# Kernel tuning notes

Hardware: AMD Instinct MI355X
Metric: run time of the kernel (lower is better)

Reference implementation:

```python
import jax, jax.numpy as jnp
import numpy as np
import math

EMBED_DIM = 1024
NUM_HEADS = 16
HEAD_DIM = EMBED_DIM // NUM_HEADS
MAX_LEN = 5000
LN_EPS = 1e-5


def _positional_encoding(max_len, embed_dim):
    pos = np.arange(max_len, dtype=np.float32)[:, None]
    div = np.exp(np.arange(0, embed_dim, 2, dtype=np.float32) * (-math.log(10000.0) / embed_dim))
    pe = np.zeros((max_len, embed_dim), dtype=np.float32)
    pe[:, 0::2] = np.sin(pos * div)
    pe[:, 1::2] = np.cos(pos * div)
    return jnp.asarray(pe)[None]  # [1, max_len, D]


def setup_inputs() -> dict:
    key = jax.random.key(0)
    ks = jax.random.split(key, 12)
    s = 1.0 / math.sqrt(EMBED_DIM)
    D = EMBED_DIM
    return {
        "x": jax.random.normal(ks[0], (4, 2048, D), dtype=jnp.float32),
        "wq": jax.random.uniform(ks[1], (D, D), jnp.float32, -s, s),
        "bq": jax.random.uniform(ks[2], (D,), jnp.float32, -s, s),
        "wk": jax.random.uniform(ks[3], (D, D), jnp.float32, -s, s),
        "bk": jax.random.uniform(ks[4], (D,), jnp.float32, -s, s),
        "wv": jax.random.uniform(ks[5], (D, D), jnp.float32, -s, s),
        "bv": jax.random.uniform(ks[6], (D,), jnp.float32, -s, s),
        "wo": jax.random.uniform(ks[7], (D, D), jnp.float32, -s, s),
        "bo": jax.random.uniform(ks[8], (D,), jnp.float32, -s, s),
        "gamma": jnp.ones((D,), jnp.float32),
        "beta": jnp.zeros((D,), jnp.float32),
        "pe": _positional_encoding(MAX_LEN, D),
    }


def reference(x, wq, bq, wk, bk, wv, bv, wo, bo, gamma, beta, pe):
    B, S, D = x.shape
    H, Hd = NUM_HEADS, HEAD_DIM
    x = x + pe[:, :S, :]
    # projections; weights stored as [in, out]
    q = (x @ wq + bq).reshape(B, S, H, Hd).transpose(0, 2, 1, 3)
    k = (x @ wk + bk).reshape(B, S, H, Hd).transpose(0, 2, 1, 3)
    v = (x @ wv + bv).reshape(B, S, H, Hd).transpose(0, 2, 1, 3)
    scores = jnp.einsum("bhqd,bhkd->bhqk", q, k) / math.sqrt(Hd)
    attn = jax.nn.softmax(scores, axis=-1)  # dropout is identity in eval
    out = jnp.einsum("bhqk,bhkd->bhqd", attn, v)
    out = out.transpose(0, 2, 1, 3).reshape(B, S, D)
    out = out @ wo + bo
    # residual + layernorm
    h = out + x
    mu = jnp.mean(h, axis=-1, keepdims=True)
    var = jnp.var(h, axis=-1, keepdims=True)
    return (h - mu) * jax.lax.rsqrt(var + LN_EPS) * gamma + beta
```

## Files before the change

kernel.cpp:

```cpp
#include <hip/hip_runtime.h>

#define DEV __device__ __forceinline__

typedef __attribute__((ext_vector_type(4))) float floatx4;
typedef __attribute__((ext_vector_type(8))) short short8;

DEV unsigned short f2bf(float f) {
  unsigned u = __float_as_uint(f);
  u += 0x7FFF + ((u >> 16) & 1);
  return (unsigned short)(u >> 16);
}
DEV float bf2f(unsigned short h) { return __uint_as_float(((unsigned)h) << 16); }

DEV unsigned pkbf(float lo, float hi) {
  return __builtin_amdgcn_perm(__float_as_uint(hi) + 0x8000u,
                               __float_as_uint(lo) + 0x8000u, 0x07060302u);
}

#if __has_builtin(__builtin_amdgcn_exp2f)
#define EXP2(x) __builtin_amdgcn_exp2f(x)
#else
#define EXP2(x) exp2f(x)
#endif

#define GLD16(g, l)                                                            \
  __builtin_amdgcn_global_load_lds(                                            \
      (const __attribute__((address_space(1))) void*)(g),                      \
      (__attribute__((address_space(3))) void*)(l), 16, 0, 0)

__global__ void k_prep(const float* __restrict__ x, const float* __restrict__ pe,
                       const float* __restrict__ w0, const float* __restrict__ w1,
                       const float* __restrict__ w2, const float* __restrict__ w3,
                       unsigned short* __restrict__ wt, float* __restrict__ xf,
                       unsigned short* __restrict__ xb) {
  __shared__ float t[64][65];
  const int bid = blockIdx.x, tid = threadIdx.x;
  if (bid < 1024) {
    const int z = bid >> 8, rem = bid & 255;
    const int bx = rem & 15, by = rem >> 4;
    const int tx = tid & 63, ty = tid >> 6;
    const float* wsel = (z == 0) ? w0 : (z == 1) ? w1 : (z == 2) ? w2 : w3;
    unsigned short* out = wt + (size_t)z * 1048576;
    const int k0 = bx * 64, n0 = by * 64;
    for (int i = ty; i < 64; i += 4)
      t[i][tx] = wsel[(size_t)(k0 + i) * 1024 + n0 + tx];
    __syncthreads();
    for (int i = ty; i < 64; i += 4)
      out[(size_t)(n0 + i) * 1024 + k0 + tx] = f2bf(t[tx][i]);
  } else {
    const int idx = (bid - 1024) * 256 + tid;
    const int row = idx >> 8;
    const int c4 = idx & 255;
    const int s = row & 2047;
    const float4 xv = ((const float4*)x)[idx];
    const float4 pv = ((const float4*)pe)[s * 256 + c4];
    float4 r;
    r.x = xv.x + pv.x; r.y = xv.y + pv.y; r.z = xv.z + pv.z; r.w = xv.w + pv.w;
    ((float4*)xf)[idx] = r;
    ushort4 o;
    o.x = f2bf(r.x); o.y = f2bf(r.y); o.z = f2bf(r.z); o.w = f2bf(r.w);
    ((ushort4*)xb)[idx] = o;
  }
}

#define GEMM_CORE(Aptr, Bptr, RB, CB)                                          \
  for (int k0 = 0; k0 < 1024; k0 += 64) {                                      \
    _Pragma("unroll") for (int r = 0; r < 4; ++r) {                            \
      const int c = r * 256 + tid;                                             \
      const int rw = c >> 3;                                                   \
      const int gc = ((c & 7) ^ (rw & 7)) << 3;                                \
      GLD16((Aptr) + (size_t)((RB) + rw) * 1024 + k0 + gc,                     \
            As + (size_t)(r * 256 + wave * 64) * 8);                           \
      GLD16((Bptr) + (size_t)((CB) + rw) * 1024 + k0 + gc,                     \
            Bs + (size_t)(r * 256 + wave * 64) * 8);                           \
    }                                                                          \
    __syncthreads();                                                           \
    _Pragma("unroll") for (int kk = 0; kk < 2; ++kk) {                         \
      short8 fa[4], fb[4];                                                     \
      _Pragma("unroll") for (int i = 0; i < 4; ++i) {                          \
        fa[i] = *(const short8*)(As + (wm * 64 + i * 16 + l16) * 64 +          \
                                 (((kk * 4 + quad) ^ (l16 & 7)) << 3));        \
        fb[i] = *(const short8*)(Bs + (wn * 64 + i * 16 + l16) * 64 +          \
                                 (((kk * 4 + quad) ^ (l16 & 7)) << 3));        \
      }                                                                        \
      _Pragma("unroll") for (int mi = 0; mi < 4; ++mi)                         \
          _Pragma("unroll") for (int ni = 0; ni < 4; ++ni) acc[mi][ni] =       \
          __builtin_amdgcn_mfma_f32_16x16x32_bf16(fa[mi], fb[ni],              \
                                                  acc[mi][ni], 0, 0, 0);       \
    }                                                                          \
    __syncthreads();                                                           \
  }

__global__ __launch_bounds__(256, 4) void k_gemmqkvt(
    const unsigned short* __restrict__ xpeb, const unsigned short* __restrict__ wt,
    const float* __restrict__ bqp, const float* __restrict__ bkp,
    const float* __restrict__ bvp, unsigned short* __restrict__ qb,
    unsigned short* __restrict__ kb, unsigned short* __restrict__ vtb) {
  __shared__ unsigned short As[128 * 64];
  __shared__ unsigned short Bs[128 * 64];
  const int tid = threadIdx.x;
  const int lane = tid & 63, wave = tid >> 6;
  const int quad = lane >> 4, l16 = lane & 15;
  const int wm = wave >> 1, wn = wave & 1;
  const int id = blockIdx.x;

  floatx4 acc[4][4];
  const floatx4 vzero = {0.f, 0.f, 0.f, 0.f};
#pragma unroll
  for (int i = 0; i < 4; ++i)
#pragma unroll
    for (int j = 0; j < 4; ++j) acc[i][j] = vzero;

  if (id < 1024) {
    const int xcd = id & 7, j = id >> 3;
    const int bx = (xcd << 3) | (j & 7), by = j >> 3;
    const int rb = bx * 128, cb = by * 128;
    GEMM_CORE(xpeb, wt, rb, cb);
    const int which = cb >> 10;
    const float* bias = (which == 0) ? bqp : bkp;
    unsigned short* out = (which == 0) ? qb : kb;
#pragma unroll
    for (int ni = 0; ni < 4; ++ni) {
      const int col = cb + wn * 64 + ni * 16 + l16;
      const int cl = col & 1023;
      const float bvv = bias[cl];
      const int h = cl >> 6, d = cl & 63;
#pragma unroll
      for (int mi = 0; mi < 4; ++mi) {
#pragma unroll
        for (int r = 0; r < 4; ++r) {
          const int row = rb + wm * 64 + mi * 16 + quad * 4 + r;
          const int b = row >> 11, s = row & 2047;
          out[((size_t)(b * 16 + h) * 2048 + s) * 64 + d] = f2bf(acc[mi][ni][r] + bvv);
        }
      }
    }
  } else {
    const int id2 = id - 1024;
    const int xcd = id2 & 7, j = id2 >> 3;
    const int by = (xcd << 3) | (j & 7), bx = j >> 3;
    const int rb = bx * 128, cb = by * 128;
    GEMM_CORE(wt + 2097152, xpeb, rb, cb);
#pragma unroll
    for (int mi = 0; mi < 4; ++mi) {
#pragma unroll
      for (int r = 0; r < 4; ++r) {
        const int row = rb + wm * 64 + mi * 16 + quad * 4 + r;
        const float bvv = bvp[row];
#pragma unroll
        for (int ni = 0; ni < 4; ++ni) {
          const int col = cb + wn * 64 + ni * 16 + l16;
          vtb[((size_t)(col >> 11) * 1024 + row) * 2048 + (col & 2047)] =
              f2bf(acc[mi][ni][r] + bvv);
        }
      }
    }
  }
}

__global__ __launch_bounds__(256, 4) void k_gemmo(
    const unsigned short* __restrict__ A, const unsigned short* __restrict__ Bt,
    const float* __restrict__ bias, unsigned short* __restrict__ out) {
  __shared__ unsigned short As[128 * 64];
  __shared__ unsigned short Bs[128 * 64];
  const int tid = threadIdx.x;
  const int lane = tid & 63, wave = tid >> 6;
  const int quad = lane >> 4, l16 = lane & 15;
  const int wm = wave >> 1, wn = wave & 1;
  const int id = blockIdx.x;
  const int xcd = id & 7, j = id >> 3;
  const int bx = (xcd << 3) | (j & 7), by = j >> 3;
  const int rb = bx * 128, cb = by * 128;

  floatx4 acc[4][4];
  const floatx4 vzero = {0.f, 0.f, 0.f, 0.f};
#pragma unroll
  for (int i = 0; i < 4; ++i)
#pragma unroll
    for (int jj = 0; jj < 4; ++jj) acc[i][jj] = vzero;

  GEMM_CORE(A, Bt, rb, cb);

#pragma unroll
  for (int ni = 0; ni < 4; ++ni) {
    const int col = cb + wn * 64 + ni * 16 + l16;
    const float bvv = bias[col];
#pragma unroll
    for (int mi = 0; mi < 4; ++mi) {
#pragma unroll
      for (int r = 0; r < 4; ++r) {
        const int row = rb + wm * 64 + mi * 16 + quad * 4 + r;
        out[(size_t)row * 1024 + col] = f2bf(acc[mi][ni][r] + bvv);
      }
    }
  }
}

__global__ __launch_bounds__(256, 4) void k_flash(
    const unsigned short* __restrict__ Q, const unsigned short* __restrict__ Kb,
    const unsigned short* __restrict__ Vt, unsigned short* __restrict__ AO) {
  __shared__ unsigned short Ks[64 * 64];
  __shared__ unsigned short Vs[64 * 64];
  __shared__ unsigned short Ps[4][32 * 72];
  const int tid = threadIdx.x, lane = tid & 63, wave = tid >> 6;
  const int quad = lane >> 4, l16 = lane & 15;
  const int g = blockIdx.x;
  const int li = g >> 3;
  const int bh = (g & 7) * 8 + (li >> 4);
  const int qt = li & 15;
  const int b = bh >> 4, h = bh & 15;

  const unsigned short* Kh = Kb + (size_t)bh * 2048 * 64;
  const unsigned short* Vh = Vt + (size_t)bh * 64 * 2048;

  const float LAMBDA = 0.125f * 1.4426950408889634f;
  short8 aq[2][2];
  {
    const unsigned short* Qb = Q + ((size_t)bh * 2048 + qt * 128 + wave * 32) * 64;
#pragma unroll
    for (int qi = 0; qi < 2; ++qi)
#pragma unroll
      for (int c = 0; c < 2; ++c) {
        const short8 raw =
            *(const short8*)(Qb + (size_t)(qi * 16 + l16) * 64 + c * 32 + quad * 8);
        short8 sv;
#pragma unroll
        for (int j = 0; j < 8; ++j)
          sv[j] = (short)f2bf(bf2f((unsigned short)raw[j]) * LAMBDA);
        aq[qi][c] = sv;
      }
  }

  short8 onesv;
#pragma unroll
  for (int j = 0; j < 8; ++j) onesv[j] = (short)0x3F80;

  const floatx4 vzero = {0.f, 0.f, 0.f, 0.f};
  floatx4 o[2][4];
#pragma unroll
  for (int qi = 0; qi < 2; ++qi)
#pragma unroll
    for (int di = 0; di < 4; ++di) o[qi][di] = vzero;
  floatx4 lacc[2] = {vzero, vzero};
  unsigned short* Pw = Ps[wave];

#define STAGE(ktile)                                                           \
  {                                                                            \
    _Pragma("unroll") for (int r = 0; r < 2; ++r) {                            \
      const int c = r * 256 + tid;                                             \
      const int rw = c >> 3;                                                   \
      const int gc = ((c & 7) ^ (rw & 7)) * 8;                                 \
      GLD16(Kh + (size_t)((ktile) * 64 + rw) * 64 + gc,                        \
            &Ks[(size_t)(r * 256 + wave * 64) * 8]);                           \
      GLD16(Vh + (size_t)rw * 2048 + (ktile) * 64 + gc,                        \
            &Vs[(size_t)(r * 256 + wave * 64) * 8]);                           \
    }                                                                          \
  }

  STAGE(0);
  __syncthreads();

  for (int kt = 0; kt < 32; ++kt) {
    short8 fk[4][2];
#pragma unroll
    for (int ni = 0; ni < 4; ++ni)
#pragma unroll
      for (int c = 0; c < 2; ++c)
        fk[ni][c] = *(const short8*)(&Ks[(ni * 16 + l16) * 64 +
                                         (((c * 4 + quad) ^ (l16 & 7)) << 3)]);

#pragma unroll
    for (int qi = 0; qi < 2; ++qi) {
      floatx4 p[4];
#pragma unroll
      for (int ni = 0; ni < 4; ++ni) {
        floatx4 t = vzero;
#pragma unroll
        for (int c = 0; c < 2; ++c)
          t = __builtin_amdgcn_mfma_f32_16x16x32_bf16(fk[ni][c], aq[qi][c], t, 0, 0, 0);
        p[ni] = t;
      }
#pragma unroll
      for (int ni = 0; ni < 4; ++ni)
#pragma unroll
        for (int r = 0; r < 4; ++r) p[ni][r] = EXP2(p[ni][r]);
#pragma unroll
      for (int ni = 0; ni < 4; ++ni) {
        uint2 pk;
        pk.x = pkbf(p[ni][0], p[ni][1]);
        pk.y = pkbf(p[ni][2], p[ni][3]);
        *(uint2*)(&Pw[(qi * 16 + l16) * 72 + ni * 16 + quad * 4]) = pk;
      }
    }
    asm volatile("s_waitcnt lgkmcnt(0)" ::: "memory");

#pragma unroll
    for (int c = 0; c < 2; ++c) {
      short8 ap[2];
#pragma unroll
      for (int qi = 0; qi < 2; ++qi)
        ap[qi] = *(const short8*)(&Pw[(qi * 16 + l16) * 72 + c * 32 + quad * 8]);
#pragma unroll
      for (int qi = 0; qi < 2; ++qi)
        lacc[qi] = __builtin_amdgcn_mfma_f32_16x16x32_bf16(ap[qi], onesv, lacc[qi], 0, 0, 0);
#pragma unroll
      for (int di = 0; di < 4; ++di) {
        const short8 fv = *(const short8*)(&Vs[(di * 16 + l16) * 64 +
                                               (((c * 4 + quad) ^ (l16 & 7)) << 3)]);
#pragma unroll
        for (int qi = 0; qi < 2; ++qi)
          o[qi][di] = __builtin_amdgcn_mfma_f32_16x16x32_bf16(ap[qi], fv, o[qi][di], 0, 0, 0);
      }
    }
    __syncthreads();
    if (kt + 1 < 32) STAGE(kt + 1);
    __syncthreads();
  }

#pragma unroll
  for (int qi = 0; qi < 2; ++qi) {
    float invl[4];
#pragma unroll
    for (int r = 0; r < 4; ++r) invl[r] = __builtin_amdgcn_rcpf(lacc[qi][r]);
#pragma unroll
    for (int di = 0; di < 4; ++di) {
#pragma unroll
      for (int r = 0; r < 4; ++r) {
        const int s = qt * 128 + wave * 32 + qi * 16 + quad * 4 + r;
        const int col = h * 64 + di * 16 + l16;
        AO[((size_t)b * 2048 + s) * 1024 + col] = f2bf(o[qi][di][r] * invl[r]);
      }
    }
  }
#undef STAGE
}

__global__ __launch_bounds__(256) void k_ln(
    const unsigned short* __restrict__ proj, const float* __restrict__ xpe,
    const float* __restrict__ gamma, const float* __restrict__ beta,
    float* __restrict__ out) {
  const int row = blockIdx.x, tid = threadIdx.x;
  const int lane = tid & 63, wave = tid >> 6;
  const float4 xv = ((const float4*)(xpe + (size_t)row * 1024))[tid];
  const ushort4 pv = ((const ushort4*)(proj + (size_t)row * 1024))[tid];
  const float h0 = xv.x + bf2f(pv.x);
  const float h1 = xv.y + bf2f(pv.y);
  const float h2 = xv.z + bf2f(pv.z);
  const float h3 = xv.w + bf2f(pv.w);
  float s = h0 + h1 + h2 + h3;
  float s2 = h0 * h0 + h1 * h1 + h2 * h2 + h3 * h3;
#pragma unroll
  for (int m = 1; m < 64; m <<= 1) {
    s += __shfl_xor(s, m);
    s2 += __shfl_xor(s2, m);
  }
  __shared__ float rs[4], rq[4];
  if (lane == 0) { rs[wave] = s; rq[wave] = s2; }
  __syncthreads();
  s = rs[0] + rs[1] + rs[2] + rs[3];
  s2 = rq[0] + rq[1] + rq[2] + rq[3];
  const float mu = s * (1.f / 1024.f);
  const float var = s2 * (1.f / 1024.f) - mu * mu;
  const float rstd = rsqrtf(var + 1e-5f);
  const float4 gv = ((const float4*)gamma)[tid];
  const float4 bvv = ((const float4*)beta)[tid];
  float4 ov;
  ov.x = (h0 - mu) * rstd * gv.x + bvv.x;
  ov.y = (h1 - mu) * rstd * gv.y + bvv.y;
  ov.z = (h2 - mu) * rstd * gv.z + bvv.z;
  ov.w = (h3 - mu) * rstd * gv.w + bvv.w;
  ((float4*)(out + (size_t)row * 1024))[tid] = ov;
}

extern "C" void kernel_launch(void* const* d_in, const int* in_sizes, int n_in,
                              void* d_out, int out_size, void* d_ws, size_t ws_size,
                              hipStream_t stream) {
  const float* x = (const float*)d_in[0];
  const float* wq = (const float*)d_in[1];
  const float* bq = (const float*)d_in[2];
  const float* wk = (const float*)d_in[3];
  const float* bk = (const float*)d_in[4];
  const float* wv = (const float*)d_in[5];
  const float* bv = (const float*)d_in[6];
  const float* wo = (const float*)d_in[7];
  const float* bo = (const float*)d_in[8];
  const float* gamma = (const float*)d_in[9];
  const float* beta = (const float*)d_in[10];
  const float* pe = (const float*)d_in[11];

  if (ws_size < 125829120) return;

  char* w = (char*)d_ws;
  unsigned short* wt = (unsigned short*)(w);
  float* xpef = (float*)(w + 8388608);
  unsigned short* xpeb = (unsigned short*)(w + 41943040);
  unsigned short* qb = (unsigned short*)(w + 58720256);
  unsigned short* kb = (unsigned short*)(w + 75497472);
  unsigned short* vtb = (unsigned short*)(w + 92274688);
  unsigned short* aob = (unsigned short*)(w + 109051904);
  unsigned short* projb = qb;

  k_prep<<<9216, 256, 0, stream>>>(x, pe, wq, wk, wv, wo, wt, xpef, xpeb);
  k_gemmqkvt<<<1536, 256, 0, stream>>>(xpeb, wt, bq, bk, bv, qb, kb, vtb);
  k_flash<<<1024, 256, 0, stream>>>(qb, kb, vtb, aob);
  k_gemmo<<<512, 256, 0, stream>>>(aob, wt + 3145728, bo, projb);
  k_ln<<<8192, 256, 0, stream>>>(projb, xpef, gamma, beta, (float*)d_out);
}
```

Before: 303.4 us.

## Double per-block tile height in QKV GEMM and flash attention kernels

The QKV projection GEMM moves from 128x128 to 256x128 output tiles, with each wave holding 8x4 accumulator fragments, and the grid shrinks from 1536 to 768 blocks. The flash attention kernel gives each wave 64 query rows instead of 32, so every staged K/V tile is shared by twice as many queries, and the grid halves to 512 blocks. The aim is to cut global and LDS traffic per FLOP and amortise more MFMA work per load. In exchange, register use and LDS per block rise, launch bounds drop to 2 blocks per CU, and the smaller grids reduce occupancy and the number of waves available to hide latency.

```diff
diff --git a/kernel.cpp b/kernel.cpp
--- a/kernel.cpp
+++ b/kernel.cpp
@@ -91,12 +91,45 @@
     __syncthreads();                                                           \
   }
 
-__global__ __launch_bounds__(256, 4) void k_gemmqkvt(
+#define GEMM_CORE_V3(Aptr, Bptr, RB, CB)                                       \
+  for (int k0 = 0; k0 < 1024; k0 += 64) {                                      \
+    _Pragma("unroll") for (int r = 0; r < 8; ++r) {                            \
+      const int c = r * 256 + tid;                                             \
+      const int rw = c >> 3;                                                   \
+      const int gc = ((c & 7) ^ (rw & 7)) << 3;                                \
+      GLD16((Aptr) + (size_t)((RB) + rw) * 1024 + k0 + gc,                     \
+            As + (size_t)(r * 256 + wave * 64) * 8);                           \
+    }                                                                          \
+    _Pragma("unroll") for (int r = 0; r < 4; ++r) {                            \
+      const int c = r * 256 + tid;                                             \
+      const int rw = c >> 3;                                                   \
+      const int gc = ((c & 7) ^ (rw & 7)) << 3;                                \
+      GLD16((Bptr) + (size_t)((CB) + rw) * 1024 + k0 + gc,                     \
+            Bs + (size_t)(r * 256 + wave * 64) * 8);                           \
+    }                                                                          \
+    __syncthreads();                                                           \
+    _Pragma("unroll") for (int kk = 0; kk < 2; ++kk) {                         \
+      short8 fa[8], fb[4];                                                     \
+      _Pragma("unroll") for (int i = 0; i < 8; ++i)                            \
+        fa[i] = *(const short8*)(As + (wm * 128 + i * 16 + l16) * 64 +         \
+                                 (((kk * 4 + quad) ^ (l16 & 7)) << 3));        \
+      _Pragma("unroll") for (int i = 0; i < 4; ++i)                            \
+        fb[i] = *(const short8*)(Bs + (wn * 64 + i * 16 + l16) * 64 +          \
+                                 (((kk * 4 + quad) ^ (l16 & 7)) << 3));        \
+      _Pragma("unroll") for (int mi = 0; mi < 8; ++mi)                         \
+          _Pragma("unroll") for (int ni = 0; ni < 4; ++ni) acc[mi][ni] =       \
+          __builtin_amdgcn_mfma_f32_16x16x32_bf16(fa[mi], fb[ni],              \
+                                                  acc[mi][ni], 0, 0, 0);       \
+    }                                                                          \
+    __syncthreads();                                                           \
+  }
+
+__global__ __launch_bounds__(256, 2) void k_gemmqkvt(
     const unsigned short* __restrict__ xpeb, const unsigned short* __restrict__ wt,
     const float* __restrict__ bqp, const float* __restrict__ bkp,
     const float* __restrict__ bvp, unsigned short* __restrict__ qb,
     unsigned short* __restrict__ kb, unsigned short* __restrict__ vtb) {
-  __shared__ unsigned short As[128 * 64];
+  __shared__ unsigned short As[256 * 64];
   __shared__ unsigned short Bs[128 * 64];
   const int tid = threadIdx.x;
   const int lane = tid & 63, wave = tid >> 6;
@@ -104,18 +137,18 @@
   const int wm = wave >> 1, wn = wave & 1;
   const int id = blockIdx.x;
 
-  floatx4 acc[4][4];
+  floatx4 acc[8][4];
   const floatx4 vzero = {0.f, 0.f, 0.f, 0.f};
 #pragma unroll
-  for (int i = 0; i < 4; ++i)
+  for (int i = 0; i < 8; ++i)
 #pragma unroll
     for (int j = 0; j < 4; ++j) acc[i][j] = vzero;
 
-  if (id < 1024) {
+  if (id < 512) {
     const int xcd = id & 7, j = id >> 3;
-    const int bx = (xcd << 3) | (j & 7), by = j >> 3;
-    const int rb = bx * 128, cb = by * 128;
-    GEMM_CORE(xpeb, wt, rb, cb);
+    const int bx = (xcd << 2) | (j & 3), by = j >> 2;
+    const int rb = bx * 256, cb = by * 128;
+    GEMM_CORE_V3(xpeb, wt, rb, cb);
     const int which = cb >> 10;
     const float* bias = (which == 0) ? bqp : bkp;
     unsigned short* out = (which == 0) ? qb : kb;
@@ -126,26 +159,26 @@
       const float bvv = bias[cl];
       const int h = cl >> 6, d = cl & 63;
 #pragma unroll
-      for (int mi = 0; mi < 4; ++mi) {
+      for (int mi = 0; mi < 8; ++mi) {
 #pragma unroll
         for (int r = 0; r < 4; ++r) {
-          const int row = rb + wm * 64 + mi * 16 + quad * 4 + r;
+          const int row = rb + wm * 128 + mi * 16 + quad * 4 + r;
           const int b = row >> 11, s = row & 2047;
           out[((size_t)(b * 16 + h) * 2048 + s) * 64 + d] = f2bf(acc[mi][ni][r] + bvv);
         }
       }
     }
   } else {
-    const int id2 = id - 1024;
+    const int id2 = id - 512;
     const int xcd = id2 & 7, j = id2 >> 3;
     const int by = (xcd << 3) | (j & 7), bx = j >> 3;
-    const int rb = bx * 128, cb = by * 128;
-    GEMM_CORE(wt + 2097152, xpeb, rb, cb);
-#pragma unroll
-    for (int mi = 0; mi < 4; ++mi) {
+    const int rb = bx * 256, cb = by * 128;
+    GEMM_CORE_V3(wt + 2097152, xpeb, rb, cb);
+#pragma unroll
+    for (int mi = 0; mi < 8; ++mi) {
 #pragma unroll
       for (int r = 0; r < 4; ++r) {
-        const int row = rb + wm * 64 + mi * 16 + quad * 4 + r;
+        const int row = rb + wm * 128 + mi * 16 + quad * 4 + r;
         const float bvv = bvp[row];
 #pragma unroll
         for (int ni = 0; ni < 4; ++ni) {
@@ -196,29 +229,29 @@
   }
 }
 
-__global__ __launch_bounds__(256, 4) void k_flash(
+__global__ __launch_bounds__(256, 2) void k_flash(
     const unsigned short* __restrict__ Q, const unsigned short* __restrict__ Kb,
     const unsigned short* __restrict__ Vt, unsigned short* __restrict__ AO) {
   __shared__ unsigned short Ks[64 * 64];
   __shared__ unsigned short Vs[64 * 64];
-  __shared__ unsigned short Ps[4][32 * 72];
+  __shared__ unsigned short Ps[4][64 * 72];
   const int tid = threadIdx.x, lane = tid & 63, wave = tid >> 6;
   const int quad = lane >> 4, l16 = lane & 15;
   const int g = blockIdx.x;
   const int li = g >> 3;
-  const int bh = (g & 7) * 8 + (li >> 4);
-  const int qt = li & 15;
+  const int bh = (g & 7) * 8 + (li >> 3);
+  const int qt = li & 7;
   const int b = bh >> 4, h = bh & 15;
 
   const unsigned short* Kh = Kb + (size_t)bh * 2048 * 64;
   const unsigned short* Vh = Vt + (size_t)bh * 64 * 2048;
 
   const float LAMBDA = 0.125f * 1.4426950408889634f;
-  short8 aq[2][2];
+  short8 aq[4][2];
   {
-    const unsigned short* Qb = Q + ((size_t)bh * 2048 + qt * 128 + wave * 32) * 64;
-#pragma unroll
-    for (int qi = 0; qi < 2; ++qi)
+    const unsigned short* Qb = Q + ((size_t)bh * 2048 + qt * 256 + wave * 64) * 64;
+#pragma unroll
+    for (int qi = 0; qi < 4; ++qi)
 #pragma unroll
       for (int c = 0; c < 2; ++c) {
         const short8 raw =
@@ -236,12 +269,12 @@
   for (int j = 0; j < 8; ++j) onesv[j] = (short)0x3F80;
 
   const floatx4 vzero = {0.f, 0.f, 0.f, 0.f};
-  floatx4 o[2][4];
-#pragma unroll
-  for (int qi = 0; qi < 2; ++qi)
+  floatx4 o[4][4];
+#pragma unroll
+  for (int qi = 0; qi < 4; ++qi)
 #pragma unroll
     for (int di = 0; di < 4; ++di) o[qi][di] = vzero;
-  floatx4 lacc[2] = {vzero, vzero};
+  floatx4 lacc[4] = {vzero, vzero, vzero, vzero};
   unsigned short* Pw = Ps[wave];
 
 #define STAGE(ktile)                                                           \
@@ -270,7 +303,7 @@
                                          (((c * 4 + quad) ^ (l16 & 7)) << 3)]);
 
 #pragma unroll
-    for (int qi = 0; qi < 2; ++qi) {
+    for (int qi = 0; qi < 4; ++qi) {
       floatx4 p[4];
 #pragma unroll
       for (int ni = 0; ni < 4; ++ni) {
@@ -296,19 +329,19 @@
 
 #pragma unroll
     for (int c = 0; c < 2; ++c) {
-      short8 ap[2];
-#pragma unroll
-      for (int qi = 0; qi < 2; ++qi)
+      short8 ap[4];
+#pragma unroll
+      for (int qi = 0; qi < 4; ++qi)
         ap[qi] = *(const short8*)(&Pw[(qi * 16 + l16) * 72 + c * 32 + quad * 8]);
 #pragma unroll
-      for (int qi = 0; qi < 2; ++qi)
+      for (int qi = 0; qi < 4; ++qi)
         lacc[qi] = __builtin_amdgcn_mfma_f32_16x16x32_bf16(ap[qi], onesv, lacc[qi], 0, 0, 0);
 #pragma unroll
       for (int di = 0; di < 4; ++di) {
         const short8 fv = *(const short8*)(&Vs[(di * 16 + l16) * 64 +
                                                (((c * 4 + quad) ^ (l16 & 7)) << 3)]);
 #pragma unroll
-        for (int qi = 0; qi < 2; ++qi)
+        for (int qi = 0; qi < 4; ++qi)
           o[qi][di] = __builtin_amdgcn_mfma_f32_16x16x32_bf16(ap[qi], fv, o[qi][di], 0, 0, 0);
       }
     }
@@ -318,7 +351,7 @@
   }
 
 #pragma unroll
-  for (int qi = 0; qi < 2; ++qi) {
+  for (int qi = 0; qi < 4; ++qi) {
     float invl[4];
 #pragma unroll
     for (int r = 0; r < 4; ++r) invl[r] = __builtin_amdgcn_rcpf(lacc[qi][r]);
@@ -326,7 +359,7 @@
     for (int di = 0; di < 4; ++di) {
 #pragma unroll
       for (int r = 0; r < 4; ++r) {
-        const int s = qt * 128 + wave * 32 + qi * 16 + quad * 4 + r;
+        const int s = qt * 256 + wave * 64 + qi * 16 + quad * 4 + r;
         const int col = h * 64 + di * 16 + l16;
         AO[((size_t)b * 2048 + s) * 1024 + col] = f2bf(o[qi][di][r] * invl[r]);
       }
@@ -401,8 +434,8 @@
   unsigned short* projb = qb;
 
   k_prep<<<9216, 256, 0, stream>>>(x, pe, wq, wk, wv, wo, wt, xpef, xpeb);
-  k_gemmqkvt<<<1536, 256, 0, stream>>>(xpeb, wt, bq, bk, bv, qb, kb, vtb);
-  k_flash<<<1024, 256, 0, stream>>>(qb, kb, vtb, aob);
+  k_gemmqkvt<<<768, 256, 0, stream>>>(xpeb, wt, bq, bk, bv, qb, kb, vtb);
+  k_flash<<<512, 256, 0, stream>>>(qb, kb, vtb, aob);
   k_gemmo<<<512, 256, 0, stream>>>(aob, wt + 3145728, bo, projb);
   k_ln<<<8192, 256, 0, stream>>>(projb, xpef, gamma, beta, (float*)d_out);
 }
```

After: 304.1 us. About the same (+0.2%).
